# Kernel tuning notes

Measured on AMD Instinct MI355X. Metric: run time of the kernel, lower is better.

The kernel has to match this reference:

```python
import jax, jax.numpy as jnp
import numpy as np

B = 8192          # number of analysis windows
N = 4096          # window_size (power of 2, matches radix-2 Cooley-Tukey)


def setup_inputs() -> dict:
    key = jax.random.key(0)
    x = jax.random.normal(key, (B, N), dtype=jnp.float32)
    return {"x": x}


def reference(x):
    """Power spectrum |F(k)|^2 per window.

    The original module implements an exact radix-2 DIT Cooley-Tukey FFT
    (bit-reversal permutation + log2(N) butterfly stages with twiddle
    factors exp(-2*pi*i*k/N)) and returns re^2 + im^2. That is exactly the
    unnormalized DFT, so the clean/efficient faithful form is jnp.fft.fft
    followed by squared magnitude, batched over the leading axis.
    """
    f = jnp.fft.fft(x.astype(jnp.complex64), axis=-1)  # [B, N] complex
    return (jnp.real(f) ** 2 + jnp.imag(f) ** 2).astype(x.dtype)  # [B, N]
```

## Files before the change

### kernel.cpp

```cpp
#include <hip/hip_runtime.h>
#include <math.h>

#define FFT_N   4096
#define NT      256
#define PHYS(i) ((i) + ((i) >> 4))
#define LDS_SZ  (FFT_N + FFT_N / 16)

__device__ __forceinline__ float2 cadd(float2 a, float2 b) { return make_float2(a.x + b.x, a.y + b.y); }
__device__ __forceinline__ float2 csub(float2 a, float2 b) { return make_float2(a.x - b.x, a.y - b.y); }
__device__ __forceinline__ float2 cmul(float2 a, float2 b) { return make_float2(a.x * b.x - a.y * b.y, a.x * b.y + a.y * b.x); }

__device__ __forceinline__ void dft4(float2& a, float2& b, float2& c, float2& d) {
    float2 t0 = cadd(a, c);
    float2 t1 = csub(a, c);
    float2 t2 = cadd(b, d);
    float2 t3 = make_float2(b.y - d.y, d.x - b.x);
    a = cadd(t0, t2);
    b = cadd(t1, t3);
    c = csub(t0, t2);
    d = csub(t1, t3);
}

__device__ __forceinline__ void dft16(float2 v[16]) {
    #pragma unroll
    for (int r1 = 0; r1 < 4; ++r1)
        dft4(v[r1], v[r1 + 4], v[r1 + 8], v[r1 + 12]);

    const float C1 = 0.92387953251128675613f;
    const float S1 = 0.38268343236508977173f;
    const float R2 = 0.70710678118654752440f;
    v[5]  = cmul(v[5],  make_float2( C1, -S1));
    v[9]  = cmul(v[9],  make_float2( R2, -R2));
    v[13] = cmul(v[13], make_float2( S1, -C1));
    v[6]  = cmul(v[6],  make_float2( R2, -R2));
    v[10] = make_float2(v[10].y, -v[10].x);
    v[14] = cmul(v[14], make_float2(-R2, -R2));
    v[7]  = cmul(v[7],  make_float2( S1, -C1));
    v[11] = cmul(v[11], make_float2(-R2, -R2));
    v[15] = cmul(v[15], make_float2(-C1,  S1));
    #pragma unroll
    for (int q1 = 0; q1 < 4; ++q1)
        dft4(v[4 * q1], v[4 * q1 + 1], v[4 * q1 + 2], v[4 * q1 + 3]);
}

template <int M>
__device__ __forceinline__ void fft_stage(float2* buf, int tid) {
    const int j = tid / M;
    const int k = tid % M;
    float2 v[16];
    #pragma unroll
    for (int r = 0; r < 16; ++r) v[r] = buf[PHYS(tid + 256 * r)];
    __syncthreads();

    dft16(v);

    const float base = (float)j * (-6.28318530717958647692f * (float)M / (float)FFT_N);
    const int obase = j * 16 * M + k;
    #pragma unroll
    for (int q = 0; q < 16; ++q) {
        const int reg = ((q & 3) << 2) | (q >> 2);
        float2 d = v[reg];
        if (M != 256 && q != 0) {
            float sn, cs;
            __sincosf(base * (float)q, &sn, &cs);
            d = make_float2(d.x * cs - d.y * sn, d.x * sn + d.y * cs);
        }
        buf[PHYS(obase + q * M)] = d;
    }
    __syncthreads();
}

__global__ __launch_bounds__(NT) void spec_fft_kernel(const float* __restrict__ x,
                                                      float* __restrict__ out) {
    __shared__ float2 buf[LDS_SZ];
    const int tid = threadIdx.x;
    const size_t base = (size_t)blockIdx.x * (2 * FFT_N);
    const float4* __restrict__ x1 = (const float4*)(x + base);
    const float4* __restrict__ x2 = (const float4*)(x + base + FFT_N);

    #pragma unroll
    for (int it = 0; it < 4; ++it) {
        int idx = tid + 256 * it;
        float4 a = x1[idx];
        float4 b = x2[idx];
        buf[PHYS(4 * idx + 0)] = make_float2(a.x, b.x);
        buf[PHYS(4 * idx + 1)] = make_float2(a.y, b.y);
        buf[PHYS(4 * idx + 2)] = make_float2(a.z, b.z);
        buf[PHYS(4 * idx + 3)] = make_float2(a.w, b.w);
    }
    __syncthreads();

    fft_stage<1>(buf, tid);
    fft_stage<16>(buf, tid);
    fft_stage<256>(buf, tid);

    float* __restrict__ o1 = out + base;
    float* __restrict__ o2 = out + base + FFT_N;
    #pragma unroll
    for (int it = 0; it < 4; ++it) {
        int idx = tid + 256 * it;
        float4 r1, r2;
        #pragma unroll
        for (int c = 0; c < 4; ++c) {
            int k = 4 * idx + c;
            float2 zk = buf[PHYS(k)];
            float2 zn = buf[PHYS((FFT_N - k) & (FFT_N - 1))];
            float e1r = zk.x + zn.x, e1i = zk.y - zn.y;
            float e2r = zk.x - zn.x, e2i = zk.y + zn.y;
            (&r1.x)[c] = 0.25f * (e1r * e1r + e1i * e1i);
            (&r2.x)[c] = 0.25f * (e2r * e2r + e2i * e2i);
        }
        ((float4*)o1)[idx] = r1;
        ((float4*)o2)[idx] = r2;
    }
}

extern "C" void kernel_launch(void* const* d_in, const int* in_sizes, int n_in,
                              void* d_out, int out_size, void* d_ws, size_t ws_size,
                              hipStream_t stream) {
    const float* x = (const float*)d_in[0];
    float* out = (float*)d_out;
    const int B = in_sizes[0] / FFT_N;
    spec_fft_kernel<<<B / 2, NT, 0, stream>>>(x, out);
}
```

Before: 49.12 us.

## Load first FFT stage directly from global and use twiddle recurrence

The input staging through LDS is removed: each thread now reads its sixteen strided elements straight from global memory into registers and runs the first radix-16 pass right away, which saves one LDS write/read round trip and a barrier. Twiddles are now generated by repeatedly multiplying one sincos result instead of calling sincos fifteen times per thread. The global loads become scalar, coalesced across threads, rather than float4. The recurrence accumulates a small rounding error over fifteen steps.

Result: slower. 50.31 us (+2.4%).

```diff
diff --git a/kernel.cpp b/kernel.cpp
--- a/kernel.cpp
+++ b/kernel.cpp
@@ -43,31 +43,35 @@
         dft4(v[4 * q1], v[4 * q1 + 1], v[4 * q1 + 2], v[4 * q1 + 3]);
 }
 
-template <int M>
-__device__ __forceinline__ void fft_stage(float2* buf, int tid) {
+template <int M, bool TW>
+__device__ __forceinline__ void store_stage(float2* buf, int tid, float2 v[16]) {
     const int j = tid / M;
     const int k = tid % M;
-    float2 v[16];
+    const int obase = j * 16 * M + k;
+    if (TW) {
+        float sn, cs;
+        __sincosf((float)j * (-6.28318530717958647692f * (float)M / (float)FFT_N), &sn, &cs);
+        const float2 w1 = make_float2(cs, sn);
+        float2 wq = w1;
+        buf[PHYS(obase)] = v[0];
+        #pragma unroll
+        for (int q = 1; q < 16; ++q) {
+            const int reg = ((q & 3) << 2) | (q >> 2);
+            buf[PHYS(obase + q * M)] = cmul(v[reg], wq);
+            wq = cmul(wq, w1);
+        }
+    } else {
+        #pragma unroll
+        for (int q = 0; q < 16; ++q) {
+            const int reg = ((q & 3) << 2) | (q >> 2);
+            buf[PHYS(obase + q * M)] = v[reg];
+        }
+    }
+}
+
+__device__ __forceinline__ void load_stage(const float2* buf, int tid, float2 v[16]) {
     #pragma unroll
     for (int r = 0; r < 16; ++r) v[r] = buf[PHYS(tid + 256 * r)];
-    __syncthreads();
-
-    dft16(v);
-
-    const float base = (float)j * (-6.28318530717958647692f * (float)M / (float)FFT_N);
-    const int obase = j * 16 * M + k;
-    #pragma unroll
-    for (int q = 0; q < 16; ++q) {
-        const int reg = ((q & 3) << 2) | (q >> 2);
-        float2 d = v[reg];
-        if (M != 256 && q != 0) {
-            float sn, cs;
-            __sincosf(base * (float)q, &sn, &cs);
-            d = make_float2(d.x * cs - d.y * sn, d.x * sn + d.y * cs);
-        }
-        buf[PHYS(obase + q * M)] = d;
-    }
-    __syncthreads();
 }
 
 __global__ __launch_bounds__(NT) void spec_fft_kernel(const float* __restrict__ x,
@@ -75,24 +79,29 @@
     __shared__ float2 buf[LDS_SZ];
     const int tid = threadIdx.x;
     const size_t base = (size_t)blockIdx.x * (2 * FFT_N);
-    const float4* __restrict__ x1 = (const float4*)(x + base);
-    const float4* __restrict__ x2 = (const float4*)(x + base + FFT_N);
+    const float* __restrict__ x1 = x + base + tid;
+    const float* __restrict__ x2 = x + base + FFT_N + tid;
 
+    float2 v[16];
     #pragma unroll
-    for (int it = 0; it < 4; ++it) {
-        int idx = tid + 256 * it;
-        float4 a = x1[idx];
-        float4 b = x2[idx];
-        buf[PHYS(4 * idx + 0)] = make_float2(a.x, b.x);
-        buf[PHYS(4 * idx + 1)] = make_float2(a.y, b.y);
-        buf[PHYS(4 * idx + 2)] = make_float2(a.z, b.z);
-        buf[PHYS(4 * idx + 3)] = make_float2(a.w, b.w);
-    }
+    for (int r = 0; r < 16; ++r)
+        v[r] = make_float2(x1[256 * r], x2[256 * r]);
+
+    dft16(v);
+    store_stage<1, true>(buf, tid, v);
     __syncthreads();
 
-    fft_stage<1>(buf, tid);
-    fft_stage<16>(buf, tid);
-    fft_stage<256>(buf, tid);
+    load_stage(buf, tid, v);
+    __syncthreads();
+    dft16(v);
+    store_stage<16, true>(buf, tid, v);
+    __syncthreads();
+
+    load_stage(buf, tid, v);
+    __syncthreads();
+    dft16(v);
+    store_stage<256, false>(buf, tid, v);
+    __syncthreads();
 
     float* __restrict__ o1 = out + base;
     float* __restrict__ o2 = out + base + FFT_N;
```
